# Performance work log

Measured on AMD Instinct MI355X. Metric: run time of the kernel, lower is better.

## Reference

```python
import jax, jax.numpy as jnp
import numpy as np


def setup_inputs() -> dict:
    key = jax.random.key(0)
    k1, k2, k3, k4 = jax.random.split(key, 4)
    B, n_env, in_ch, out_ch, code_ch, modes1, L = 16, 8, 32, 32, 16, 64, 8192
    scale = 1.0 / (in_ch * out_ch)
    return {
        "x": jax.random.normal(k1, (B, n_env * in_ch, L), dtype=jnp.float32),
        "codes": jax.random.normal(k2, (n_env, code_ch), dtype=jnp.float32),
        "com_weights": scale * jax.random.uniform(k3, (in_ch, out_ch, modes1, 2), dtype=jnp.float32),
        "code_weights": scale * jax.random.uniform(k4, (code_ch * in_ch, out_ch, modes1, 2), dtype=jnp.float32),
        "filter_weights": -3.0 * jnp.ones((modes1,), dtype=jnp.float32),
    }


def _as_complex(w):
    return w[..., 0] + 1j * w[..., 1]


def reference(x, codes, com_weights, code_weights, filter_weights):
    B, C, L = x.shape
    n_env, code_ch = codes.shape
    in_ch = C // n_env
    out_ch = com_weights.shape[1]
    modes1 = com_weights.shape[2]
    n_freq = L // 2 + 1

    # FFT and reshape to [B, e, i, freq]
    x_ft = jnp.fft.rfft(x).reshape(B, n_env, in_ch, n_freq)
    xm = x_ft[..., :modes1]  # mode truncation

    cw = _as_complex(com_weights)  # [i, o, m]
    codew = _as_complex(code_weights.reshape(code_ch, in_ch, out_ch, modes1, 2))  # [c,i,o,m]
    env_w = jnp.einsum('ec,ciom->eiom', codes.astype(codew.dtype), codew)

    # hardsigmoid(filter_weights): clip(x/6 + 0.5, 0, 1)
    lam = jnp.clip(filter_weights / 6.0 + 0.5, 0.0, 1.0)  # [m]

    out_m = (lam * jnp.einsum('beim,iom->beom', xm, cw)
             + (1.0 - lam) * jnp.einsum('beim,eiom->beom', xm, env_w))  # [B,e,o,m]

    # zero-pad back to full spectrum then inverse FFT
    out_ft = jnp.zeros((B, n_env, out_ch, n_freq), dtype=out_m.dtype)
    out_ft = out_ft.at[..., :modes1].set(out_m)
    out_ft = out_ft.reshape(B, n_env * out_ch, n_freq)
    return jnp.fft.irfft(out_ft, n=L)
```

## Files before the change

### kernel.cpp

```cpp
#include <hip/hip_runtime.h>
#include <hip/hip_bf16.h>
#include <math.h>
#include <stdint.h>

typedef __bf16 bf16_t;
typedef __bf16 bf16x8 __attribute__((ext_vector_type(8)));
typedef float  f32x4  __attribute__((ext_vector_type(4)));

#define L_LEN 8192
#define MODES 64
#define NCOMP 128
#define M_ROWS 4096
#define SPLITS 16

__device__ __forceinline__ void g2lds16(const void* g, void* l) {
  __builtin_amdgcn_global_load_lds(
      (__attribute__((address_space(1))) void*)(uintptr_t)(g),
      (__attribute__((address_space(3))) void*)(l), 16, 0, 0);
}

__global__ __launch_bounds__(256) void prep(bf16_t* __restrict__ B1t,
                                            bf16_t* __restrict__ B1,
                                            const float* __restrict__ codes,
                                            const float* __restrict__ comw,
                                            const float* __restrict__ codew,
                                            const float* __restrict__ fw,
                                            float* __restrict__ W) {
  const float C0 = 7.6699039394282061e-4f;
  if (blockIdx.x < 512) {
    const int id = blockIdx.x * 256 + threadIdx.x;
    if (id < 65536) {
      const int l8 = id & 1023, k = id >> 10;
      const int l0 = l8 * 8;
      bf16x8 vc, vs;
#pragma unroll
      for (int j = 0; j < 8; ++j) {
        int r = ((l0 + j) * k) & (L_LEN - 1);
        float s, c;
        __sincosf((float)r * C0, &s, &c);
        vc[j] = (bf16_t)c;
        vs[j] = (bf16_t)(-s);
      }
      *(bf16x8*)(B1t + (size_t)k * L_LEN + l0)           = vc;
      *(bf16x8*)(B1t + (size_t)(MODES + k) * L_LEN + l0) = vs;
    } else {
      const int id2 = id - 65536;
      const int k8 = id2 & 7, l = id2 >> 3;
      const int kk = k8 * 8;
      bf16x8 vc, vs;
#pragma unroll
      for (int j = 0; j < 8; ++j) {
        int r = (l * (kk + j)) & (L_LEN - 1);
        float s, c;
        __sincosf((float)r * C0, &s, &c);
        vc[j] = (bf16_t)c;
        vs[j] = (bf16_t)(-s);
      }
      *(bf16x8*)(B1 + (size_t)l * NCOMP + kk)         = vc;
      *(bf16x8*)(B1 + (size_t)l * NCOMP + MODES + kk) = vs;
    }
  } else {
    int id = (blockIdx.x - 512) * 256 + threadIdx.x;
    int k = id & 63;
    int o = (id >> 6) & 31;
    int i = (id >> 11) & 31;
    int e = id >> 16;
    float lam = fminf(fmaxf(fw[k] * (1.0f / 6.0f) + 0.5f, 0.0f), 1.0f);
    float are = 0.f, aim = 0.f;
#pragma unroll
    for (int c = 0; c < 16; ++c) {
      float cd = codes[e * 16 + c];
      const float* p = codew + ((((c * 32 + i) * 32 + o) * 64 + k) << 1);
      are += cd * p[0];
      aim += cd * p[1];
    }
    const float* q = comw + (((i * 32 + o) * 64 + k) << 1);
    float wre = lam * q[0] + (1.f - lam) * are;
    float wim = lam * q[1] + (1.f - lam) * aim;
    float* dst = W + ((((e * 32 + i) * 32 + o) * 64 + k) << 1);
    dst[0] = wre;
    dst[1] = wim;
  }
}

__global__ __launch_bounds__(256, 4) void stage1(const float* __restrict__ x,
                                                 const bf16_t* __restrict__ B1t,
                                                 float* __restrict__ Xp) {
  __shared__ bf16_t Bs[2][128 * 64];
  const int t = threadIdx.x;
  const int lane = t & 63;
  const int w = t >> 6;
  const int l15 = lane & 15, lq = lane >> 4;
  const int m0 = blockIdx.x * 64 + w * 16;
  const int k0 = blockIdx.y * 512;

  const float* aptr = x + (size_t)(m0 + l15) * L_LEN + k0 + lq * 8;

#pragma unroll
  for (int q = 0; q < 4; ++q) {
    int slot = t + 256 * q;
    int n = slot >> 3, m8 = slot & 7, j8 = m8 ^ (n & 7);
    g2lds16(B1t + (size_t)n * L_LEN + k0 + j8 * 8, (char*)(&Bs[0][0]) + slot * 16);
  }
  float4 pa0 = *(const float4*)(aptr + 0);
  float4 pa1 = *(const float4*)(aptr + 4);
  float4 pa2 = *(const float4*)(aptr + 32);
  float4 pa3 = *(const float4*)(aptr + 36);

  f32x4 acc[8];
#pragma unroll
  for (int nf = 0; nf < 8; ++nf) acc[nf] = (f32x4){0.f, 0.f, 0.f, 0.f};

#pragma unroll
  for (int ch = 0; ch < 8; ++ch) {
    float4 a0 = pa0, a1 = pa1, a2 = pa2, a3 = pa3;
    if (ch < 7) {
#pragma unroll
      for (int q = 0; q < 4; ++q) {
        int slot = t + 256 * q;
        int n = slot >> 3, m8 = slot & 7, j8 = m8 ^ (n & 7);
        g2lds16(B1t + (size_t)n * L_LEN + k0 + (ch + 1) * 64 + j8 * 8,
                (char*)(&Bs[(ch + 1) & 1][0]) + slot * 16);
      }
      const float* ap2 = aptr + (ch + 1) * 64;
      pa0 = *(const float4*)(ap2 + 0);
      pa1 = *(const float4*)(ap2 + 4);
      pa2 = *(const float4*)(ap2 + 32);
      pa3 = *(const float4*)(ap2 + 36);
      asm volatile("s_waitcnt vmcnt(8)" ::: "memory");
    } else {
      asm volatile("s_waitcnt vmcnt(0)" ::: "memory");
    }
    __builtin_amdgcn_s_barrier();
    asm volatile("" ::: "memory");
    bf16x8 av0 = {(bf16_t)a0.x, (bf16_t)a0.y, (bf16_t)a0.z, (bf16_t)a0.w,
                  (bf16_t)a1.x, (bf16_t)a1.y, (bf16_t)a1.z, (bf16_t)a1.w};
    bf16x8 av1 = {(bf16_t)a2.x, (bf16_t)a2.y, (bf16_t)a2.z, (bf16_t)a2.w,
                  (bf16_t)a3.x, (bf16_t)a3.y, (bf16_t)a3.z, (bf16_t)a3.w};
    const bf16_t* bb = &Bs[ch & 1][0];
#pragma unroll
    for (int s = 0; s < 2; ++s) {
      bf16x8 av = s ? av1 : av0;
#pragma unroll
      for (int nf = 0; nf < 8; ++nf) {
        int n = nf * 16 + l15;
        int j8 = (s * 4 + lq) ^ (n & 7);
        bf16x8 bv = *(const bf16x8*)(bb + n * 64 + j8 * 8);
        acc[nf] = __builtin_amdgcn_mfma_f32_16x16x32_bf16(bv, av, acc[nf], 0, 0, 0);
      }
    }
    if (ch < 7) __builtin_amdgcn_s_barrier();
  }

  float* xout = Xp + (size_t)blockIdx.y * (M_ROWS * NCOMP) +
                (size_t)(m0 + l15) * NCOMP + lq * 4;
#pragma unroll
  for (int nf = 0; nf < 8; ++nf)
    *(float4*)(xout + nf * 16) = (float4){acc[nf][0], acc[nf][1], acc[nf][2], acc[nf][3]};
}

__global__ __launch_bounds__(256) void mixk(const float* __restrict__ Xp,
                                            const float* __restrict__ W,
                                            bf16_t* __restrict__ A2) {
  __shared__ __align__(16) float Xs[32 * 128];
  const int t = threadIdx.x;
  const int be = blockIdx.x;
  const int oh = blockIdx.y;
  const int e = be & 7;
  const float* xb = Xp + (size_t)be * (32 * NCOMP);
#pragma unroll
  for (int j = 0; j < 4; ++j) {
    int idx = (t + 256 * j) * 4;
    f32x4 s = (f32x4){0.f, 0.f, 0.f, 0.f};
#pragma unroll
    for (int sp = 0; sp < 16; ++sp)
      s += *(const f32x4*)(xb + (size_t)sp * (M_ROWS * NCOMP) + idx);
    *(f32x4*)(Xs + idx) = s;
  }
  __syncthreads();
  const int k = t & 63;
  const int olo = t >> 6;
  float yre[4], yim[4];
#pragma unroll
  for (int j = 0; j < 4; ++j) { yre[j] = 0.f; yim[j] = 0.f; }
  for (int i = 0; i < 32; ++i) {
    float xr = Xs[i * 128 + k];
    float xi = Xs[i * 128 + 64 + k];
    const float* wp = W + ((((e * 32 + i) * 32 + olo * 8 + oh * 4) * 64 + k) << 1);
#pragma unroll
    for (int j = 0; j < 4; ++j) {
      float2 wv = *(const float2*)(wp + j * 128);
      yre[j] += xr * wv.x - xi * wv.y;
      yim[j] += xr * wv.y + xi * wv.x;
    }
  }
  float sc = (k == 0) ? (1.0f / 8192.0f) : (2.0f / 8192.0f);
#pragma unroll
  for (int j = 0; j < 4; ++j) {
    int m = be * 32 + olo * 8 + oh * 4 + j;
    A2[m * NCOMP + k]         = (bf16_t)(yre[j] * sc);
    A2[m * NCOMP + MODES + k] = (bf16_t)(yim[j] * sc);
  }
}

__global__ __launch_bounds__(256) void stage2(const bf16_t* __restrict__ A2,
                                              const bf16_t* __restrict__ B1,
                                              float* __restrict__ out) {
  __shared__ bf16_t Bs[128 * 128];
  const int t = threadIdx.x;
  const int lane = t & 63;
  const int w = t >> 6;
  const int l15 = lane & 15, lq = lane >> 4;
  const int m0 = blockIdx.x * 64 + w * 16;
  const int l0 = blockIdx.y * 128;

#pragma unroll
  for (int q = 0; q < 8; ++q) {
    int slot = t + 256 * q;
    int lr = slot >> 4, m16 = slot & 15, j8 = m16 ^ (lr & 15);
    g2lds16(B1 + (size_t)(l0 + lr) * NCOMP + j8 * 8, (char*)Bs + slot * 16);
  }
  const bf16_t* ap = A2 + (size_t)(m0 + l15) * NCOMP + lq * 8;
  bf16x8 av[4];
#pragma unroll
  for (int s = 0; s < 4; ++s) av[s] = *(const bf16x8*)(ap + s * 32);

  f32x4 acc[8];
#pragma unroll
  for (int nf = 0; nf < 8; ++nf) acc[nf] = (f32x4){0.f, 0.f, 0.f, 0.f};

  __syncthreads();

#pragma unroll
  for (int s = 0; s < 4; ++s) {
#pragma unroll
    for (int nf = 0; nf < 8; ++nf) {
      int lr = nf * 16 + l15;
      int j8 = (s * 4 + lq) ^ (lr & 15);
      bf16x8 bv = *(const bf16x8*)(Bs + lr * 128 + j8 * 8);
      acc[nf] = __builtin_amdgcn_mfma_f32_16x16x32_bf16(bv, av[s], acc[nf], 0, 0, 0);
    }
  }

  float* op = out + (size_t)(m0 + l15) * L_LEN + l0 + lq * 4;
#pragma unroll
  for (int nf = 0; nf < 8; ++nf)
    *(float4*)(op + nf * 16) = (float4){acc[nf][0], acc[nf][1], acc[nf][2], acc[nf][3]};
}

extern "C" void kernel_launch(void* const* d_in, const int* in_sizes, int n_in,
                              void* d_out, int out_size, void* d_ws, size_t ws_size,
                              hipStream_t stream) {
  const float* x     = (const float*)d_in[0];
  const float* codes = (const float*)d_in[1];
  const float* comw  = (const float*)d_in[2];
  const float* codew = (const float*)d_in[3];
  const float* fw    = (const float*)d_in[4];
  float* out = (float*)d_out;
  char* ws = (char*)d_ws;
  bf16_t* B1t = (bf16_t*)(ws);
  bf16_t* B1  = (bf16_t*)(ws + (size_t)(2u << 20));
  float*  W   = (float*) (ws + (size_t)(4u << 20));
  bf16_t* A2  = (bf16_t*)(ws + (size_t)(20u << 20));
  float*  Xp  = (float*) (ws + (size_t)(24u << 20));

  prep<<<2560, 256, 0, stream>>>(B1t, B1, codes, comw, codew, fw, W);
  stage1<<<dim3(64, SPLITS), 256, 0, stream>>>(x, B1t, Xp);
  mixk<<<dim3(128, 2), 256, 0, stream>>>(Xp, W, A2);
  stage2<<<dim3(64, 64), 256, 0, stream>>>(A2, B1, out);
}
```

Before: 301.1 us.

## Vectorize weight-mix prep, split mixk by mode halves, add MFMA priority hints

The prep weight-mixing branch now has each thread handle two modes with 16-byte vector loads and stores, which halves that part's grid. mixk is repartitioned so each block reduces only half of the mode columns from the split-K partials, rather than every block reducing all 128 columns. This removes the duplicated partial-sum reads across the two blocks per row. Stage1 and stage2 wrap their MFMA loops in s_setprio to favour waves that are issuing matrix ops. Together these aim to cut redundant global traffic and scheduling stalls, at the cost of narrower per-block work in mixk.

```diff
diff --git a/kernel.cpp b/kernel.cpp
--- a/kernel.cpp
+++ b/kernel.cpp
@@ -61,25 +61,26 @@
     }
   } else {
     int id = (blockIdx.x - 512) * 256 + threadIdx.x;
-    int k = id & 63;
-    int o = (id >> 6) & 31;
-    int i = (id >> 11) & 31;
-    int e = id >> 16;
-    float lam = fminf(fmaxf(fw[k] * (1.0f / 6.0f) + 0.5f, 0.0f), 1.0f);
-    float are = 0.f, aim = 0.f;
+    int kp = id & 31;
+    int o = (id >> 5) & 31;
+    int i = (id >> 10) & 31;
+    int e = id >> 15;
+    float lam0 = fminf(fmaxf(fw[2 * kp]     * (1.0f / 6.0f) + 0.5f, 0.0f), 1.0f);
+    float lam1 = fminf(fmaxf(fw[2 * kp + 1] * (1.0f / 6.0f) + 0.5f, 0.0f), 1.0f);
+    f32x4 a = (f32x4){0.f, 0.f, 0.f, 0.f};
 #pragma unroll
     for (int c = 0; c < 16; ++c) {
       float cd = codes[e * 16 + c];
-      const float* p = codew + ((((c * 32 + i) * 32 + o) * 64 + k) << 1);
-      are += cd * p[0];
-      aim += cd * p[1];
-    }
-    const float* q = comw + (((i * 32 + o) * 64 + k) << 1);
-    float wre = lam * q[0] + (1.f - lam) * are;
-    float wim = lam * q[1] + (1.f - lam) * aim;
-    float* dst = W + ((((e * 32 + i) * 32 + o) * 64 + k) << 1);
-    dst[0] = wre;
-    dst[1] = wim;
+      f32x4 p = *(const f32x4*)(codew + ((((c * 32 + i) * 32 + o) * 64) << 1) + kp * 4);
+      a += cd * p;
+    }
+    f32x4 q = *(const f32x4*)(comw + (((i * 32 + o) * 64) << 1) + kp * 4);
+    f32x4 r;
+    r[0] = lam0 * q[0] + (1.f - lam0) * a[0];
+    r[1] = lam0 * q[1] + (1.f - lam0) * a[1];
+    r[2] = lam1 * q[2] + (1.f - lam1) * a[2];
+    r[3] = lam1 * q[3] + (1.f - lam1) * a[3];
+    *(f32x4*)(W + ((((e * 32 + i) * 32 + o) * 64) << 1) + kp * 4) = r;
   }
 }
 
@@ -138,6 +139,7 @@
     bf16x8 av1 = {(bf16_t)a2.x, (bf16_t)a2.y, (bf16_t)a2.z, (bf16_t)a2.w,
                   (bf16_t)a3.x, (bf16_t)a3.y, (bf16_t)a3.z, (bf16_t)a3.w};
     const bf16_t* bb = &Bs[ch & 1][0];
+    __builtin_amdgcn_s_setprio(1);
 #pragma unroll
     for (int s = 0; s < 2; ++s) {
       bf16x8 av = s ? av1 : av0;
@@ -149,6 +151,7 @@
         acc[nf] = __builtin_amdgcn_mfma_f32_16x16x32_bf16(bv, av, acc[nf], 0, 0, 0);
       }
     }
+    __builtin_amdgcn_s_setprio(0);
     if (ch < 7) __builtin_amdgcn_s_barrier();
   }
 
@@ -162,31 +165,36 @@
 __global__ __launch_bounds__(256) void mixk(const float* __restrict__ Xp,
                                             const float* __restrict__ W,
                                             bf16_t* __restrict__ A2) {
-  __shared__ __align__(16) float Xs[32 * 128];
+  __shared__ __align__(16) float Xs[32 * 64];
   const int t = threadIdx.x;
   const int be = blockIdx.x;
-  const int oh = blockIdx.y;
+  const int kh = blockIdx.y;
   const int e = be & 7;
+  const int cb = kh * 32;
   const float* xb = Xp + (size_t)be * (32 * NCOMP);
 #pragma unroll
-  for (int j = 0; j < 4; ++j) {
-    int idx = (t + 256 * j) * 4;
+  for (int j = 0; j < 2; ++j) {
+    int qid = t + 256 * j;
+    int row = qid >> 4, sub = qid & 15;
+    int col  = (sub < 8) ? (cb + sub * 4) : (64 + cb + (sub - 8) * 4);
+    int scol = (sub < 8) ? (sub * 4)      : (32 + (sub - 8) * 4);
     f32x4 s = (f32x4){0.f, 0.f, 0.f, 0.f};
 #pragma unroll
     for (int sp = 0; sp < 16; ++sp)
-      s += *(const f32x4*)(xb + (size_t)sp * (M_ROWS * NCOMP) + idx);
-    *(f32x4*)(Xs + idx) = s;
+      s += *(const f32x4*)(xb + (size_t)sp * (M_ROWS * NCOMP) + row * NCOMP + col);
+    *(f32x4*)(Xs + row * 64 + scol) = s;
   }
   __syncthreads();
-  const int k = t & 63;
-  const int olo = t >> 6;
+  const int kb = t & 31;
+  const int k = cb + kb;
+  const int grp = t >> 5;
   float yre[4], yim[4];
 #pragma unroll
   for (int j = 0; j < 4; ++j) { yre[j] = 0.f; yim[j] = 0.f; }
   for (int i = 0; i < 32; ++i) {
-    float xr = Xs[i * 128 + k];
-    float xi = Xs[i * 128 + 64 + k];
-    const float* wp = W + ((((e * 32 + i) * 32 + olo * 8 + oh * 4) * 64 + k) << 1);
+    float xr = Xs[i * 64 + kb];
+    float xi = Xs[i * 64 + 32 + kb];
+    const float* wp = W + ((((e * 32 + i) * 32 + grp * 4) * 64 + k) << 1);
 #pragma unroll
     for (int j = 0; j < 4; ++j) {
       float2 wv = *(const float2*)(wp + j * 128);
@@ -197,7 +205,7 @@
   float sc = (k == 0) ? (1.0f / 8192.0f) : (2.0f / 8192.0f);
 #pragma unroll
   for (int j = 0; j < 4; ++j) {
-    int m = be * 32 + olo * 8 + oh * 4 + j;
+    int m = be * 32 + grp * 4 + j;
     A2[m * NCOMP + k]         = (bf16_t)(yre[j] * sc);
     A2[m * NCOMP + MODES + k] = (bf16_t)(yim[j] * sc);
   }
@@ -231,6 +239,7 @@
 
   __syncthreads();
 
+  __builtin_amdgcn_s_setprio(1);
 #pragma unroll
   for (int s = 0; s < 4; ++s) {
 #pragma unroll
@@ -241,6 +250,7 @@
       acc[nf] = __builtin_amdgcn_mfma_f32_16x16x32_bf16(bv, av[s], acc[nf], 0, 0, 0);
     }
   }
+  __builtin_amdgcn_s_setprio(0);
 
   float* op = out + (size_t)(m0 + l15) * L_LEN + l0 + lq * 4;
 #pragma unroll
@@ -264,7 +274,7 @@
   bf16_t* A2  = (bf16_t*)(ws + (size_t)(20u << 20));
   float*  Xp  = (float*) (ws + (size_t)(24u << 20));
 
-  prep<<<2560, 256, 0, stream>>>(B1t, B1, codes, comw, codew, fw, W);
+  prep<<<1536, 256, 0, stream>>>(B1t, B1, codes, comw, codew, fw, W);
   stage1<<<dim3(64, SPLITS), 256, 0, stream>>>(x, B1t, Xp);
   mixk<<<dim3(128, 2), 256, 0, stream>>>(Xp, W, A2);
   stage2<<<dim3(64, 64), 256, 0, stream>>>(A2, B1, out);
```

After: 295.9 us. About the same (-1.7%).
